# Kernel tuning notes

Hardware: AMD Instinct MI355X
Metric: run time of the kernel (lower is better)

The kernel has to match this reference:

```python
import jax, jax.numpy as jnp
import numpy as np

B, T, H, W = 4, 32, 160, 320
NF, FPF = 8, 8          # num_filters, features_per_filter
SPEED_DIM = 8           # speed_embedding output width
U = 64                  # internal LTC neurons (wiring units)
S = NF * FPF + SPEED_DIM  # 72 sensory inputs
M = 1                   # motor (output) neurons
ODE_UNFOLDS = 6
EPS = 1e-8


def setup_inputs() -> dict:
    key = jax.random.key(0)
    k = jax.random.split(key, 20)
    f32 = jnp.float32
    sp = (H // 8) * (W // 8)  # spatial size per filter after 3 stride-2 convs = 800
    d = {}
    d["input_sequence"] = jax.random.normal(k[0], (B, T, 3, H, W), f32)
    d["speed_sequence"] = jax.random.uniform(k[1], (B, T, 1), f32)
    # conv head params
    d["conv1_w"] = jax.random.normal(k[2], (16, 3, 5, 5), f32) * 0.05
    d["conv1_b"] = jnp.zeros((16,), f32)
    d["conv2_w"] = jax.random.normal(k[3], (32, 16, 5, 5), f32) * 0.05
    d["conv2_b"] = jnp.zeros((32,), f32)
    d["conv3_w"] = jax.random.normal(k[4], (NF, 32, 5, 5), f32) * 0.05
    d["conv3_b"] = jnp.zeros((NF,), f32)
    d["head_w"] = jax.random.normal(k[5], (NF, sp, FPF), f32) * 0.02  # per-filter Linear
    d["head_b"] = jnp.zeros((NF, FPF), f32)
    # speed embedding MLP (Dropout is identity at inference)
    d["se_w1"] = jax.random.normal(k[6], (1, 16), f32) * 0.5
    d["se_b1"] = jnp.zeros((16,), f32)
    d["se_w2"] = jax.random.normal(k[7], (16, SPEED_DIM), f32) * 0.3
    d["se_b2"] = jnp.zeros((SPEED_DIM,), f32)
    # LTC cell params (ncps-style init ranges)
    d["input_w"] = jnp.ones((S,), f32)
    d["input_b"] = jnp.zeros((S,), f32)
    d["gleak"] = jax.random.uniform(k[8], (U,), f32, 0.001, 1.0)
    d["vleak"] = jax.random.uniform(k[9], (U,), f32, -0.2, 0.2)
    d["cm"] = jax.random.uniform(k[10], (U,), f32, 0.4, 0.6)
    d["sigma"] = jax.random.uniform(k[11], (U, U), f32, 3.0, 8.0)
    d["mu"] = jax.random.uniform(k[12], (U, U), f32, 0.3, 0.8)
    d["w_syn"] = jax.random.uniform(k[13], (U, U), f32, 0.001, 1.0)
    d["erev"] = jnp.asarray(jax.random.bernoulli(k[14], 0.5, (U, U)), f32) * 2.0 - 1.0
    d["sensory_sigma"] = jax.random.uniform(k[15], (S, U), f32, 3.0, 8.0)
    d["sensory_mu"] = jax.random.uniform(k[16], (S, U), f32, 0.3, 0.8)
    d["sensory_w"] = jax.random.uniform(k[17], (S, U), f32, 0.001, 1.0)
    d["sensory_erev"] = jnp.asarray(jax.random.bernoulli(k[18], 0.5, (S, U)), f32) * 2.0 - 1.0
    d["output_w"] = jnp.ones((M,), f32)
    d["output_b"] = jnp.zeros((M,), f32)
    return d


def _conv(x, w, b, stride):
    y = jax.lax.conv_general_dilated(
        x, w, (stride, stride), [(2, 2), (2, 2)],
        dimension_numbers=("NCHW", "OIHW", "NCHW"))
    return jax.nn.relu(y + b[None, :, None, None])


def reference(input_sequence, speed_sequence, conv1_w, conv1_b, conv2_w, conv2_b,
              conv3_w, conv3_b, head_w, head_b, se_w1, se_b1, se_w2, se_b2,
              input_w, input_b, gleak, vleak, cm, sigma, mu, w_syn, erev,
              sensory_sigma, sensory_mu, sensory_w, sensory_erev, output_w, output_b):
    Bv, Tv = input_sequence.shape[:2]
    # ---- conv head over all frames at once ----
    x = input_sequence.reshape(Bv * Tv, 3, H, W)
    x = _conv(x, conv1_w, conv1_b, 2)
    x = _conv(x, conv2_w, conv2_b, 2)
    x = _conv(x, conv3_w, conv3_b, 2)          # [N, NF, H/8, W/8]
    x = x.reshape(Bv * Tv, NF, -1)             # [N, NF, 800]
    feats = jnp.einsum("nfp,fpk->nfk", x, head_w) + head_b  # per-filter Linear
    feats = feats.reshape(Bv, Tv, NF * FPF)    # [B, T, 64]
    # global-std normalization (torch .std() uses ddof=1)
    feats = feats / (jnp.std(feats, ddof=1) + 1e-5)
    # ---- speed embedding (vectorized over B,T) ----
    s = speed_sequence[..., :1]                # [B, T, 1]
    emb = jnp.tanh(jax.nn.relu(s @ se_w1 + se_b1) @ se_w2 + se_b2)  # [B, T, 8]
    xs = jnp.concatenate([feats, emb], axis=-1)   # [B, T, S]
    xs = jnp.swapaxes(xs, 0, 1)                   # [T, B, S]
    cm_t = cm * ODE_UNFOLDS  # cm / (elapsed_time / ode_unfolds), elapsed_time = 1.0

    def step(v, x_t):
        inp = x_t * input_w + input_b  # affine input mapping, [B, S]
        s_act = sensory_w * jax.nn.sigmoid((inp[:, :, None] - sensory_mu) * sensory_sigma)  # [B,S,U]
        w_num_s = jnp.sum(s_act * sensory_erev, axis=1)
        w_den_s = jnp.sum(s_act, axis=1)
        for _ in range(ODE_UNFOLDS):  # semi-implicit Euler unfolds
            w_act = w_syn * jax.nn.sigmoid((v[:, :, None] - mu) * sigma)  # [B,U,U]
            w_num = jnp.sum(w_act * erev, axis=1) + w_num_s
            w_den = jnp.sum(w_act, axis=1) + w_den_s
            v = (cm_t * v + gleak * vleak + w_num) / (cm_t + gleak + w_den + EPS)
        out = v[:, :M] * output_w + output_b  # affine output mapping on motor neurons
        return v, (out, v)

    v0 = jnp.zeros((Bv, U), feats.dtype)
    v_last, (outs, hs) = jax.lax.scan(step, v0, xs)
    readout = jnp.swapaxes(outs, 0, 1)  # [B, T, M]
    all_h = jnp.swapaxes(hs, 0, 1)      # [B, T, U]
    return readout, v_last, all_h
```

## Files before the change

### kernel.cpp

```cpp
#include <hip/hip_runtime.h>
#include <math.h>

#define BB 4
#define TT 32
#define NF 8
#define FPF 8
#define SDIM 8
#define UU 64
#define SS 72
#define UNFOLDS 6

typedef short short8 __attribute__((ext_vector_type(8)));
typedef float f32x4 __attribute__((ext_vector_type(4)));
union Frag { uint4 u; short8 s; };

__device__ __forceinline__ float fast_sigmoid(float x) {
    float e = exp2f(-1.44269504f * x);
    return __builtin_amdgcn_rcpf(1.0f + e);
}

__device__ __forceinline__ ushort f2b(float f) {
    union { float f; uint u; } a;
    a.f = f;
    uint u = a.u;
    return (ushort)((u + 0x7FFFu + ((u >> 16) & 1u)) >> 16);
}

__device__ __forceinline__ float bcast_lane(float v, int lane) {
    return __uint_as_float(__builtin_amdgcn_readlane(__float_as_uint(v), lane));
}

__global__ __launch_bounds__(256) void cvt_input(const float* __restrict__ in,
                                                 ushort* __restrict__ outp) {
    int idx = blockIdx.x * 256 + threadIdx.x;
    if (idx >= 128 * 160 * 320) return;
    int x = idx % 320;
    int r = idx / 320;
    int y = r % 160;
    int n = r / 160;
    const float* base = in + ((size_t)n * 3 * 160 + y) * 320 + x;
    float c0 = base[0];
    float c1 = base[160 * 320];
    float c2 = base[2 * 160 * 320];
    uint2 pk;
    pk.x = (uint)f2b(c0) | ((uint)f2b(c1) << 16);
    pk.y = (uint)f2b(c2);
    *(uint2*)(outp + ((size_t)((n * 164 + y + 2) * 328) + (x + 2)) * 4) = pk;
}

template <int HP, int WP, int H, int W, int CH>
__device__ __forceinline__ void halo_body(ushort* __restrict__ buf, int bid) {
    constexpr int TOPBOT = 2 * WP;
    constexpr int SIDE = WP - W;
    constexpr int NH = 2 * TOPBOT + H * SIDE;
    int idx = bid * 256 + threadIdx.x;
    if (idx >= 128 * NH) return;
    int n = idx / NH;
    int h = idx - n * NH;
    int y, x;
    if (h < TOPBOT) {
        y = h / WP;
        x = h % WP;
    } else if (h < 2 * TOPBOT) {
        int hh = h - TOPBOT;
        y = H + 2 + hh / WP;
        x = hh % WP;
    } else {
        int hh = h - 2 * TOPBOT;
        y = 2 + hh / SIDE;
        int xi = hh % SIDE;
        x = (xi < 2) ? xi : (W + xi);
    }
    ushort* p = buf + (((size_t)n * HP + y) * WP + x) * CH;
    if constexpr (CH == 4) {
        *(uint2*)p = make_uint2(0u, 0u);
    } else {
        uint4 z = make_uint4(0u, 0u, 0u, 0u);
#pragma unroll
        for (int i = 0; i < CH / 8; i++) *(uint4*)(p + i * 8) = z;
    }
}
__global__ __launch_bounds__(256) void fill_halo_all(ushort* __restrict__ p1,
                                                     ushort* __restrict__ p2,
                                                     ushort* __restrict__ p3) {
    int bid = blockIdx.x;
    if (bid < 1296)
        halo_body<164, 328, 160, 320, 4>(p1, bid);
    else if (bid < 1296 + 488)
        halo_body<84, 164, 80, 160, 16>(p2, bid - 1296);
    else
        halo_body<44, 84, 40, 80, 32>(p3, bid - 1784);
}

__global__ void wswz1_kernel(const float* __restrict__ w, uint4* __restrict__ o) {
    int i = blockIdx.x * 64 + threadIdx.x;
    if (i >= 5 * 64) return;
    int lane = i & 63, s = i >> 6;
    int oc = lane & 15, q = lane >> 4;
    ushort v[8];
#pragma unroll
    for (int j = 0; j < 8; j++) {
        int k = q * 8 + j;
        int kx = k >> 2, c = k & 3;
        float f = (kx < 5 && c < 3) ? w[((oc * 3 + c) * 5 + s) * 5 + kx] : 0.f;
        v[j] = f2b(f);
    }
    uint4 u;
    u.x = (uint)v[0] | ((uint)v[1] << 16);
    u.y = (uint)v[2] | ((uint)v[3] << 16);
    u.z = (uint)v[4] | ((uint)v[5] << 16);
    u.w = (uint)v[6] | ((uint)v[7] << 16);
    o[i] = u;
}
__global__ void wswz2_kernel(const float* __restrict__ w, uint4* __restrict__ o) {
    int i = blockIdx.x * 64 + threadIdx.x;
    if (i >= 15 * 2 * 64) return;
    int lane = i & 63;
    int ct = (i >> 6) & 1;
    int s = i >> 7;
    int ky = s / 3, kxp = s % 3;
    int oc = ct * 16 + (lane & 15);
    int q = lane >> 4, h = q >> 1;
    int kx = 2 * kxp + h;
    ushort v[8];
#pragma unroll
    for (int j = 0; j < 8; j++) {
        int ch = (q & 1) * 8 + j;
        float f = (kx < 5) ? w[((oc * 16 + ch) * 5 + ky) * 5 + kx] : 0.f;
        v[j] = f2b(f);
    }
    uint4 u;
    u.x = (uint)v[0] | ((uint)v[1] << 16);
    u.y = (uint)v[2] | ((uint)v[3] << 16);
    u.z = (uint)v[4] | ((uint)v[5] << 16);
    u.w = (uint)v[6] | ((uint)v[7] << 16);
    o[i] = u;
}
__global__ void wswz3_kernel(const float* __restrict__ w, uint4* __restrict__ o) {
    int i = blockIdx.x * 64 + threadIdx.x;
    if (i >= 25 * 64) return;
    int lane = i & 63, s = i >> 6;
    int ky = s / 5, kx = s % 5;
    int oc = lane & 15, q = lane >> 4;
    ushort v[8];
#pragma unroll
    for (int j = 0; j < 8; j++) {
        int ch = q * 8 + j;
        float f = (oc < 8) ? w[((oc * 32 + ch) * 5 + ky) * 5 + kx] : 0.f;
        v[j] = f2b(f);
    }
    uint4 u;
    u.x = (uint)v[0] | ((uint)v[1] << 16);
    u.y = (uint)v[2] | ((uint)v[3] << 16);
    u.z = (uint)v[4] | ((uint)v[5] << 16);
    u.w = (uint)v[6] | ((uint)v[7] << 16);
    o[i] = u;
}

__global__ __launch_bounds__(256) void conv1_mfma(const ushort* __restrict__ inp,
                                                  const uint4* __restrict__ wswz,
                                                  const float* __restrict__ bias,
                                                  ushort* __restrict__ outp) {
    const int lane = threadIdx.x & 63;
    const int wid = threadIdx.x >> 6;
    const int col = lane & 15, q = lane >> 4;

    Frag A[5];
#pragma unroll
    for (int s = 0; s < 5; s++) A[s].u = wswz[s * 64 + lane];
    float b0 = bias[q * 4 + 0], b1 = bias[q * 4 + 1], b2 = bias[q * 4 + 2], b3 = bias[q * 4 + 3];

    int gw = blockIdx.x * 4 + wid;
#pragma unroll
    for (int t = 0; t < 4; t++) {
        int p0 = gw * 64 + t * 16;
        int n = p0 / 12800;
        int rem = p0 - n * 12800;
        int oy = rem / 160;
        int ox0 = rem - oy * 160;
        int ox = ox0 + col;
        uint e0 = ((uint)(n * 164 + oy * 2) * 328u + (uint)(ox * 2 + 2 * q)) * 4u;
        f32x4 acc = {0.f, 0.f, 0.f, 0.f};
#pragma unroll
        for (int s = 0; s < 5; s++) {
            Frag B;
            B.u = *(const uint4*)(inp + e0 + (uint)s * (328u * 4u));
            acc = __builtin_amdgcn_mfma_f32_16x16x32_bf16(A[s].s, B.s, acc, 0, 0, 0);
        }
        uint oe = ((uint)(n * 84 + oy + 2) * 164u + (uint)(ox + 2)) * 16u + q * 4u;
        uint2 pk;
        pk.x = (uint)f2b(fmaxf(acc[0] + b0, 0.f)) | ((uint)f2b(fmaxf(acc[1] + b1, 0.f)) << 16);
        pk.y = (uint)f2b(fmaxf(acc[2] + b2, 0.f)) | ((uint)f2b(fmaxf(acc[3] + b3, 0.f)) << 16);
        *(uint2*)(outp + oe) = pk;
    }
}

__global__ __launch_bounds__(256) void conv2_mfma(const ushort* __restrict__ inp,
                                                  const uint4* __restrict__ wswz,
                                                  const float* __restrict__ bias,
                                                  ushort* __restrict__ outp) {
    const int lane = threadIdx.x & 63;
    const int wid = threadIdx.x >> 6;
    const int col = lane & 15, q = lane >> 4;
    const int h = q >> 1, chh = q & 1;

    int gw = blockIdx.x * 4 + wid;
    uint eb[4];
#pragma unroll
    for (int t = 0; t < 4; t++) {
        int p0 = gw * 64 + t * 16;
        int n = p0 / 3200;
        int rem = p0 - n * 3200;
        int oy = rem / 80;
        int ox0 = rem - oy * 80;
        eb[t] = ((uint)(n * 84 + oy * 2) * 164u + (uint)((ox0 + col) * 2 + h)) * 16u + chh * 8u;
    }
    f32x4 acc[4][2];
#pragma unroll
    for (int t = 0; t < 4; t++) {
        acc[t][0] = {0.f, 0.f, 0.f, 0.f};
        acc[t][1] = {0.f, 0.f, 0.f, 0.f};
    }
#pragma unroll
    for (int s = 0; s < 15; s++) {
        const int ky = s / 3, kxp = s % 3;
        Frag A0, A1;
        A0.u = wswz[(s * 2 + 0) * 64 + lane];
        A1.u = wswz[(s * 2 + 1) * 64 + lane];
        const uint d = (uint)ky * (164u * 16u) + (uint)kxp * 32u;
#pragma unroll
        for (int t = 0; t < 4; t++) {
            Frag B;
            B.u = *(const uint4*)(inp + eb[t] + d);
            acc[t][0] = __builtin_amdgcn_mfma_f32_16x16x32_bf16(A0.s, B.s, acc[t][0], 0, 0, 0);
            acc[t][1] = __builtin_amdgcn_mfma_f32_16x16x32_bf16(A1.s, B.s, acc[t][1], 0, 0, 0);
        }
    }
    float ba[2][4];
#pragma unroll
    for (int c = 0; c < 2; c++)
#pragma unroll
        for (int r = 0; r < 4; r++) ba[c][r] = bias[c * 16 + q * 4 + r];
#pragma unroll
    for (int t = 0; t < 4; t++) {
        int p0 = gw * 64 + t * 16;
        int n = p0 / 3200;
        int rem = p0 - n * 3200;
        int oy = rem / 80;
        int ox0 = rem - oy * 80;
        int ox = ox0 + col;
        uint oe = ((uint)(n * 44 + oy + 2) * 84u + (uint)(ox + 2)) * 32u;
#pragma unroll
        for (int c = 0; c < 2; c++) {
            uint2 pk;
            pk.x = (uint)f2b(fmaxf(acc[t][c][0] + ba[c][0], 0.f)) |
                   ((uint)f2b(fmaxf(acc[t][c][1] + ba[c][1], 0.f)) << 16);
            pk.y = (uint)f2b(fmaxf(acc[t][c][2] + ba[c][2], 0.f)) |
                   ((uint)f2b(fmaxf(acc[t][c][3] + ba[c][3], 0.f)) << 16);
            *(uint2*)(outp + oe + (uint)c * 16u + (uint)q * 4u) = pk;
        }
    }
}

__global__ __launch_bounds__(256) void conv3_mfma(const ushort* __restrict__ inp,
                                                  const uint4* __restrict__ wswz,
                                                  const float* __restrict__ bias,
                                                  float* __restrict__ outp) {
    const int lane = threadIdx.x & 63;
    const int wid = threadIdx.x >> 6;
    const int col = lane & 15, q = lane >> 4;

    int gw = blockIdx.x * 4 + wid;
    uint eb[4];
#pragma unroll
    for (int t = 0; t < 4; t++) {
        int p0 = gw * 64 + t * 16;
        int n = p0 / 800;
        int pix = p0 - n * 800 + col;
        int oy = pix / 40;
        int ox = pix - oy * 40;
        eb[t] = ((uint)(n * 44 + oy * 2) * 84u + (uint)(ox * 2)) * 32u + q * 8u;
    }
    f32x4 acc[4];
#pragma unroll
    for (int t = 0; t < 4; t++) acc[t] = {0.f, 0.f, 0.f, 0.f};
#pragma unroll
    for (int s = 0; s < 25; s++) {
        const int ky = s / 5, kx = s % 5;
        Frag A;
        A.u = wswz[s * 64 + lane];
        const uint d = ((uint)ky * 84u + (uint)kx) * 32u;
#pragma unroll
        for (int t = 0; t < 4; t++) {
            Frag B;
            B.u = *(const uint4*)(inp + eb[t] + d);
            acc[t] = __builtin_amdgcn_mfma_f32_16x16x32_bf16(A.s, B.s, acc[t], 0, 0, 0);
        }
    }
    if (q < 2) {
        float b0 = bias[q * 4 + 0], b1 = bias[q * 4 + 1];
        float b2 = bias[q * 4 + 2], b3 = bias[q * 4 + 3];
#pragma unroll
        for (int t = 0; t < 4; t++) {
            int p0 = gw * 64 + t * 16;
            int n = p0 / 800;
            int p = p0 - n * 800 + col;
            float4 v;
            v.x = fmaxf(acc[t][0] + b0, 0.f);
            v.y = fmaxf(acc[t][1] + b1, 0.f);
            v.z = fmaxf(acc[t][2] + b2, 0.f);
            v.w = fmaxf(acc[t][3] + b3, 0.f);
            *(float4*)(outp + ((size_t)n * 800 + p) * 8 + q * 4) = v;
        }
    }
}

__global__ __launch_bounds__(256) void head_kernel(const float* __restrict__ x,
                                                   const float* __restrict__ hw,
                                                   const float* __restrict__ hb,
                                                   float* __restrict__ feats) {
    __shared__ float part[4][64];
    int n = blockIdx.x;
    int tid = threadIdx.x;
    int lane = tid & 63;
    int c = tid >> 6;
    int f = lane >> 3;
    int k = lane & 7;
    const float* xb = x + (size_t)n * 800 * 8 + f;
    const float* wb = hw + ((size_t)f * 800) * FPF + k;
    float acc = 0.0f;
    for (int p = c * 200; p < c * 200 + 200; p++)
        acc = fmaf(xb[(size_t)p * 8], wb[(size_t)p * FPF], acc);
    part[c][lane] = acc;
    __syncthreads();
    if (c == 0)
        feats[n * 64 + lane] = part[0][lane] + part[1][lane] + part[2][lane] + part[3][lane] +
                               hb[lane];
}

__global__ void stats_kernel(const float* __restrict__ feats, float* __restrict__ invstd) {
    __shared__ float s_sum[256], s_sq[256];
    int tid = threadIdx.x;
    float s = 0.0f, q = 0.0f;
    for (int i = tid; i < 8192; i += 256) {
        float x = feats[i];
        s += x;
        q += x * x;
    }
    s_sum[tid] = s;
    s_sq[tid] = q;
    __syncthreads();
    for (int off = 128; off > 0; off >>= 1) {
        if (tid < off) {
            s_sum[tid] += s_sum[tid + off];
            s_sq[tid] += s_sq[tid + off];
        }
        __syncthreads();
    }
    if (tid == 0) {
        float mean = s_sum[0] / 8192.0f;
        float var = (s_sq[0] - 8192.0f * mean * mean) / 8191.0f;
        var = fmaxf(var, 0.0f);
        invstd[0] = 1.0f / (sqrtf(var) + 1e-5f);
    }
}

__global__ void semb_kernel(const float* __restrict__ speed, const float* __restrict__ w1,
                            const float* __restrict__ b1, const float* __restrict__ w2,
                            const float* __restrict__ b2, float* __restrict__ emb) {
    int n = threadIdx.x;
    float s = speed[n];
    float h[16];
#pragma unroll
    for (int j = 0; j < 16; j++) h[j] = fmaxf(fmaf(s, w1[j], b1[j]), 0.0f);
#pragma unroll
    for (int k = 0; k < SDIM; k++) {
        float a = b2[k];
#pragma unroll
        for (int j = 0; j < 16; j++) a = fmaf(h[j], w2[j * SDIM + k], a);
        emb[n * SDIM + k] = tanhf(a);
    }
}

__global__ void sensory_kernel(const float* __restrict__ feats, const float* __restrict__ emb,
                               const float* __restrict__ invstd, const float* __restrict__ inw,
                               const float* __restrict__ inb, const float* __restrict__ ssig,
                               const float* __restrict__ smu, const float* __restrict__ sw,
                               const float* __restrict__ serev, float* __restrict__ wns,
                               float* __restrict__ wds) {
    int bid = blockIdx.x;
    int t = bid >> 2;
    int b = bid & 3;
    int u = threadIdx.x;
    int n = b * TT + t;
    float inv = invstd[0];
    float num = 0.0f, den = 0.0f;
    for (int s = 0; s < SS; s++) {
        float xsv = (s < 64) ? feats[n * 64 + s] * inv : emb[n * SDIM + (s - 64)];
        float inp = fmaf(xsv, inw[s], inb[s]);
        int idx = s * UU + u;
        float x = (inp - smu[idx]) * ssig[idx];
        float act = sw[idx] * fast_sigmoid(x);
        num = fmaf(act, serev[idx], num);
        den += act;
    }
    wns[bid * UU + u] = num;
    wds[bid * UU + u] = den;
}

__global__ __launch_bounds__(512, 1) void scan_kernel(
    const float* __restrict__ wns, const float* __restrict__ wds,
    const float* __restrict__ gleak, const float* __restrict__ vleak,
    const float* __restrict__ cm, const float* __restrict__ sigma,
    const float* __restrict__ mu, const float* __restrict__ wsyn,
    const float* __restrict__ erev, const float* __restrict__ outw,
    const float* __restrict__ outb, float* __restrict__ dout) {
    int b = blockIdx.x;
    int tid = threadIdx.x;
    int u = tid & 63;
    int pc_s = __builtin_amdgcn_readfirstlane(tid >> 6);

    __shared__ float2 pbuf[2][8][64];

    float sA[8], sB[8], wer[8], w_[8];
#pragma unroll
    for (int i = 0; i < 8; i++) {
        int idx = (pc_s * 8 + i) * UU + u;
        float sg = sigma[idx];
        sA[i] = -1.44269504f * sg;
        sB[i] = -sA[i] * mu[idx];
        w_[i] = wsyn[idx];
        wer[i] = w_[i] * erev[idx];
    }
#pragma unroll
    for (int i = 0; i < 8; i++) {
        asm volatile("" : "+v"(sA[i]), "+v"(sB[i]), "+v"(wer[i]), "+v"(w_[i]));
    }
    float cmt = cm[u] * (float)UNFOLDS;
    float gl = gleak[u];
    float glvl = gl * vleak[u];
    float ow = outw[0], ob = outb[0];
    float v = 0.0f;
    int par = 0;

    float num_s = wns[(0 * BB + b) * UU + u];
    float den_s = wds[(0 * BB + b) * UU + u];
    for (int t = 0; t < TT; t++) {
        float nns = 0.f, nds = 0.f;
        if (t + 1 < TT) {
            nns = wns[((t + 1) * BB + b) * UU + u];
            nds = wds[((t + 1) * BB + b) * UU + u];
        }
#pragma unroll
        for (int k = 0; k < UNFOLDS; k++) {
            float num = 0.0f, den = 0.0f;
#pragma unroll
            for (int i = 0; i < 8; i++) {
                float vi = bcast_lane(v, pc_s * 8 + i);
                float e = exp2f(fmaf(vi, sA[i], sB[i]));
                float r = __builtin_amdgcn_rcpf(1.0f + e);
                num = fmaf(wer[i], r, num);
                den = fmaf(w_[i], r, den);
            }
            pbuf[par][pc_s][u] = make_float2(num, den);
            __builtin_amdgcn_sched_barrier(0);
            asm volatile("s_waitcnt lgkmcnt(0)" ::: "memory");
            __builtin_amdgcn_s_barrier();
            asm volatile("" ::: "memory");
            __builtin_amdgcn_sched_barrier(0);
            float nn = num_s, dd = den_s;
#pragma unroll
            for (int j = 0; j < 8; j++) {
                float2 p = pbuf[par][j][u];
                nn += p.x;
                dd += p.y;
            }
            float denom = cmt + gl + dd + 1e-8f;
            v = (fmaf(cmt, v, glvl) + nn) * __builtin_amdgcn_rcpf(denom);
            par ^= 1;
        }
        if (pc_s == 0) {
            dout[384 + (b * TT + t) * UU + u] = v;
            if (u == 0) dout[b * TT + t] = fmaf(v, ow, ob);
            if (t == TT - 1) dout[128 + b * UU + u] = v;
        }
        num_s = nns;
        den_s = nds;
    }
}

extern "C" void kernel_launch(void* const* d_in, const int* in_sizes, int n_in,
                              void* d_out, int out_size, void* d_ws, size_t ws_size,
                              hipStream_t stream) {
    const float* in_seq = (const float*)d_in[0];
    const float* speed = (const float*)d_in[1];
    const float* c1w = (const float*)d_in[2];
    const float* c1b = (const float*)d_in[3];
    const float* c2w = (const float*)d_in[4];
    const float* c2b = (const float*)d_in[5];
    const float* c3w = (const float*)d_in[6];
    const float* c3b = (const float*)d_in[7];
    const float* hw = (const float*)d_in[8];
    const float* hb = (const float*)d_in[9];
    const float* sew1 = (const float*)d_in[10];
    const float* seb1 = (const float*)d_in[11];
    const float* sew2 = (const float*)d_in[12];
    const float* seb2 = (const float*)d_in[13];
    const float* inw = (const float*)d_in[14];
    const float* inb = (const float*)d_in[15];
    const float* gleak = (const float*)d_in[16];
    const float* vleak = (const float*)d_in[17];
    const float* cm = (const float*)d_in[18];
    const float* sigma = (const float*)d_in[19];
    const float* mu = (const float*)d_in[20];
    const float* wsyn = (const float*)d_in[21];
    const float* erev = (const float*)d_in[22];
    const float* ssig = (const float*)d_in[23];
    const float* smu = (const float*)d_in[24];
    const float* sw = (const float*)d_in[25];
    const float* serev = (const float*)d_in[26];
    const float* outw = (const float*)d_in[27];
    const float* outb = (const float*)d_in[28];

    char* ws = (char*)d_ws;
    float* out = (float*)d_out;

    size_t off = 0;
    auto alloc = [&](size_t bytes) {
        size_t o = off;
        off += (bytes + 255) & ~(size_t)255;
        return o;
    };
    ushort* inp1 = (ushort*)(ws + alloc((size_t)128 * 164 * 328 * 4 * 2));
    ushort* c1out = (ushort*)(ws + alloc((size_t)128 * 84 * 164 * 16 * 2));
    ushort* c2out = (ushort*)(ws + alloc((size_t)128 * 44 * 84 * 32 * 2));
    float* c3out = (float*)(ws + alloc((size_t)128 * 800 * 8 * 4));
    float* feats = (float*)(ws + alloc(8192 * 4));
    float* emb = (float*)(ws + alloc(1024 * 4));
    float* invstd = (float*)(ws + alloc(64));
    float* wns = (float*)(ws + alloc(8192 * 4));
    float* wds = (float*)(ws + alloc(8192 * 4));
    uint4* wz1 = (uint4*)(ws + alloc(5 * 64 * 16));
    uint4* wz2 = (uint4*)(ws + alloc(30 * 64 * 16));
    uint4* wz3 = (uint4*)(ws + alloc(25 * 64 * 16));

    wswz1_kernel<<<5, 64, 0, stream>>>(c1w, wz1);
    wswz2_kernel<<<30, 64, 0, stream>>>(c2w, wz2);
    wswz3_kernel<<<25, 64, 0, stream>>>(c3w, wz3);

    fill_halo_all<<<2032, 256, 0, stream>>>(inp1, c1out, c2out);
    cvt_input<<<25600, 256, 0, stream>>>(in_seq, inp1);

    conv1_mfma<<<6400, 256, 0, stream>>>(inp1, wz1, c1b, c1out);
    conv2_mfma<<<1600, 256, 0, stream>>>(c1out, wz2, c2b, c2out);
    conv3_mfma<<<400, 256, 0, stream>>>(c2out, wz3, c3b, c3out);

    head_kernel<<<128, 256, 0, stream>>>(c3out, hw, hb, feats);
    stats_kernel<<<1, 256, 0, stream>>>(feats, invstd);
    semb_kernel<<<1, 128, 0, stream>>>(speed, sew1, seb1, sew2, seb2, emb);

    sensory_kernel<<<TT * BB, 64, 0, stream>>>(feats, emb, invstd, inw, inb, ssig, smu, sw,
                                               serev, wns, wds);

    scan_kernel<<<BB, 512, 0, stream>>>(wns, wds, gleak, vleak, cm, sigma, mu, wsyn, erev,
                                        outw, outb, out);
}
```

Before: 277.2 us.

## Fuse prep kernels into one launch and fold stats/embed/sensory into scan

The weight swizzles, halo fill and input conversion now run as one prep kernel with block-range dispatch. Feature statistics, the speed embedding and the sensory synaptic sums move into the scan kernel, which computes them into shared memory before the recurrence. This cuts eight launches down to two and removes the global round-trips for the intermediate buffers. In exchange, each of the four scan blocks redundantly reduces all of feats and does the sensory work on only four blocks, which may lengthen the serial tail.

```diff
diff --git a/kernel.cpp b/kernel.cpp
--- a/kernel.cpp
+++ b/kernel.cpp
@@ -30,10 +30,8 @@
     return __uint_as_float(__builtin_amdgcn_readlane(__float_as_uint(v), lane));
 }
 
-__global__ __launch_bounds__(256) void cvt_input(const float* __restrict__ in,
-                                                 ushort* __restrict__ outp) {
-    int idx = blockIdx.x * 256 + threadIdx.x;
-    if (idx >= 128 * 160 * 320) return;
+__device__ __forceinline__ void cvt_body(const float* __restrict__ in,
+                                         ushort* __restrict__ outp, int idx) {
     int x = idx % 320;
     int r = idx / 320;
     int y = r % 160;
@@ -80,21 +78,18 @@
         for (int i = 0; i < CH / 8; i++) *(uint4*)(p + i * 8) = z;
     }
 }
-__global__ __launch_bounds__(256) void fill_halo_all(ushort* __restrict__ p1,
-                                                     ushort* __restrict__ p2,
-                                                     ushort* __restrict__ p3) {
-    int bid = blockIdx.x;
-    if (bid < 1296)
-        halo_body<164, 328, 160, 320, 4>(p1, bid);
-    else if (bid < 1296 + 488)
-        halo_body<84, 164, 80, 160, 16>(p2, bid - 1296);
-    else
-        halo_body<44, 84, 40, 80, 32>(p3, bid - 1784);
-}
-
-__global__ void wswz1_kernel(const float* __restrict__ w, uint4* __restrict__ o) {
-    int i = blockIdx.x * 64 + threadIdx.x;
-    if (i >= 5 * 64) return;
+
+__device__ __forceinline__ uint4 pack8(const ushort v[8]) {
+    uint4 u;
+    u.x = (uint)v[0] | ((uint)v[1] << 16);
+    u.y = (uint)v[2] | ((uint)v[3] << 16);
+    u.z = (uint)v[4] | ((uint)v[5] << 16);
+    u.w = (uint)v[6] | ((uint)v[7] << 16);
+    return u;
+}
+
+__device__ __forceinline__ void wswz1_body(const float* __restrict__ w, uint4* __restrict__ o,
+                                           int i) {
     int lane = i & 63, s = i >> 6;
     int oc = lane & 15, q = lane >> 4;
     ushort v[8];
@@ -105,16 +100,10 @@
         float f = (kx < 5 && c < 3) ? w[((oc * 3 + c) * 5 + s) * 5 + kx] : 0.f;
         v[j] = f2b(f);
     }
-    uint4 u;
-    u.x = (uint)v[0] | ((uint)v[1] << 16);
-    u.y = (uint)v[2] | ((uint)v[3] << 16);
-    u.z = (uint)v[4] | ((uint)v[5] << 16);
-    u.w = (uint)v[6] | ((uint)v[7] << 16);
-    o[i] = u;
-}
-__global__ void wswz2_kernel(const float* __restrict__ w, uint4* __restrict__ o) {
-    int i = blockIdx.x * 64 + threadIdx.x;
-    if (i >= 15 * 2 * 64) return;
+    o[i] = pack8(v);
+}
+__device__ __forceinline__ void wswz2_body(const float* __restrict__ w, uint4* __restrict__ o,
+                                           int i) {
     int lane = i & 63;
     int ct = (i >> 6) & 1;
     int s = i >> 7;
@@ -129,16 +118,10 @@
         float f = (kx < 5) ? w[((oc * 16 + ch) * 5 + ky) * 5 + kx] : 0.f;
         v[j] = f2b(f);
     }
-    uint4 u;
-    u.x = (uint)v[0] | ((uint)v[1] << 16);
-    u.y = (uint)v[2] | ((uint)v[3] << 16);
-    u.z = (uint)v[4] | ((uint)v[5] << 16);
-    u.w = (uint)v[6] | ((uint)v[7] << 16);
-    o[i] = u;
-}
-__global__ void wswz3_kernel(const float* __restrict__ w, uint4* __restrict__ o) {
-    int i = blockIdx.x * 64 + threadIdx.x;
-    if (i >= 25 * 64) return;
+    o[i] = pack8(v);
+}
+__device__ __forceinline__ void wswz3_body(const float* __restrict__ w, uint4* __restrict__ o,
+                                           int i) {
     int lane = i & 63, s = i >> 6;
     int ky = s / 5, kx = s % 5;
     int oc = lane & 15, q = lane >> 4;
@@ -149,12 +132,34 @@
         float f = (oc < 8) ? w[((oc * 32 + ch) * 5 + ky) * 5 + kx] : 0.f;
         v[j] = f2b(f);
     }
-    uint4 u;
-    u.x = (uint)v[0] | ((uint)v[1] << 16);
-    u.y = (uint)v[2] | ((uint)v[3] << 16);
-    u.z = (uint)v[4] | ((uint)v[5] << 16);
-    u.w = (uint)v[6] | ((uint)v[7] << 16);
-    o[i] = u;
+    o[i] = pack8(v);
+}
+
+__global__ __launch_bounds__(256) void prep_kernel(
+    const float* __restrict__ in_seq, ushort* __restrict__ inp1, ushort* __restrict__ c1out,
+    ushort* __restrict__ c2out, const float* __restrict__ c1w, const float* __restrict__ c2w,
+    const float* __restrict__ c3w, uint4* __restrict__ wz1, uint4* __restrict__ wz2,
+    uint4* __restrict__ wz3) {
+    int bid = blockIdx.x;
+    if (bid < 25600) {
+        cvt_body(in_seq, inp1, bid * 256 + threadIdx.x);
+    } else if (bid < 25600 + 2032) {
+        int hb = bid - 25600;
+        if (hb < 1296)
+            halo_body<164, 328, 160, 320, 4>(inp1, hb);
+        else if (hb < 1296 + 488)
+            halo_body<84, 164, 80, 160, 16>(c1out, hb - 1296);
+        else
+            halo_body<44, 84, 40, 80, 32>(c2out, hb - 1784);
+    } else {
+        int i = (bid - 27632) * 256 + threadIdx.x;
+        if (i < 320)
+            wswz1_body(c1w, wz1, i);
+        else if (i < 2240)
+            wswz2_body(c2w, wz2, i - 320);
+        else
+            wswz3_body(c3w, wz3, i - 2240);
+    }
 }
 
 __global__ __launch_bounds__(256) void conv1_mfma(const ushort* __restrict__ inp,
@@ -338,78 +343,13 @@
                                hb[lane];
 }
 
-__global__ void stats_kernel(const float* __restrict__ feats, float* __restrict__ invstd) {
-    __shared__ float s_sum[256], s_sq[256];
-    int tid = threadIdx.x;
-    float s = 0.0f, q = 0.0f;
-    for (int i = tid; i < 8192; i += 256) {
-        float x = feats[i];
-        s += x;
-        q += x * x;
-    }
-    s_sum[tid] = s;
-    s_sq[tid] = q;
-    __syncthreads();
-    for (int off = 128; off > 0; off >>= 1) {
-        if (tid < off) {
-            s_sum[tid] += s_sum[tid + off];
-            s_sq[tid] += s_sq[tid + off];
-        }
-        __syncthreads();
-    }
-    if (tid == 0) {
-        float mean = s_sum[0] / 8192.0f;
-        float var = (s_sq[0] - 8192.0f * mean * mean) / 8191.0f;
-        var = fmaxf(var, 0.0f);
-        invstd[0] = 1.0f / (sqrtf(var) + 1e-5f);
-    }
-}
-
-__global__ void semb_kernel(const float* __restrict__ speed, const float* __restrict__ w1,
-                            const float* __restrict__ b1, const float* __restrict__ w2,
-                            const float* __restrict__ b2, float* __restrict__ emb) {
-    int n = threadIdx.x;
-    float s = speed[n];
-    float h[16];
-#pragma unroll
-    for (int j = 0; j < 16; j++) h[j] = fmaxf(fmaf(s, w1[j], b1[j]), 0.0f);
-#pragma unroll
-    for (int k = 0; k < SDIM; k++) {
-        float a = b2[k];
-#pragma unroll
-        for (int j = 0; j < 16; j++) a = fmaf(h[j], w2[j * SDIM + k], a);
-        emb[n * SDIM + k] = tanhf(a);
-    }
-}
-
-__global__ void sensory_kernel(const float* __restrict__ feats, const float* __restrict__ emb,
-                               const float* __restrict__ invstd, const float* __restrict__ inw,
-                               const float* __restrict__ inb, const float* __restrict__ ssig,
-                               const float* __restrict__ smu, const float* __restrict__ sw,
-                               const float* __restrict__ serev, float* __restrict__ wns,
-                               float* __restrict__ wds) {
-    int bid = blockIdx.x;
-    int t = bid >> 2;
-    int b = bid & 3;
-    int u = threadIdx.x;
-    int n = b * TT + t;
-    float inv = invstd[0];
-    float num = 0.0f, den = 0.0f;
-    for (int s = 0; s < SS; s++) {
-        float xsv = (s < 64) ? feats[n * 64 + s] * inv : emb[n * SDIM + (s - 64)];
-        float inp = fmaf(xsv, inw[s], inb[s]);
-        int idx = s * UU + u;
-        float x = (inp - smu[idx]) * ssig[idx];
-        float act = sw[idx] * fast_sigmoid(x);
-        num = fmaf(act, serev[idx], num);
-        den += act;
-    }
-    wns[bid * UU + u] = num;
-    wds[bid * UU + u] = den;
-}
-
-__global__ __launch_bounds__(512, 1) void scan_kernel(
-    const float* __restrict__ wns, const float* __restrict__ wds,
+__global__ __launch_bounds__(512, 1) void scan_fused(
+    const float* __restrict__ feats, const float* __restrict__ speed,
+    const float* __restrict__ sew1, const float* __restrict__ seb1,
+    const float* __restrict__ sew2, const float* __restrict__ seb2,
+    const float* __restrict__ inw, const float* __restrict__ inb,
+    const float* __restrict__ ssig, const float* __restrict__ smu,
+    const float* __restrict__ sw, const float* __restrict__ serev,
     const float* __restrict__ gleak, const float* __restrict__ vleak,
     const float* __restrict__ cm, const float* __restrict__ sigma,
     const float* __restrict__ mu, const float* __restrict__ wsyn,
@@ -420,6 +360,9 @@
     int u = tid & 63;
     int pc_s = __builtin_amdgcn_readfirstlane(tid >> 6);
 
+    __shared__ float2 red[512];
+    __shared__ float2 sens[TT][UU];
+    __shared__ float embsh[TT][SDIM];
     __shared__ float2 pbuf[2][8][64];
 
     float sA[8], sB[8], wer[8], w_[8];
@@ -436,6 +379,61 @@
     for (int i = 0; i < 8; i++) {
         asm volatile("" : "+v"(sA[i]), "+v"(sB[i]), "+v"(wer[i]), "+v"(w_[i]));
     }
+
+    float s = 0.0f, q = 0.0f;
+    for (int i = tid; i < 8192; i += 512) {
+        float x = feats[i];
+        s += x;
+        q += x * x;
+    }
+    red[tid] = make_float2(s, q);
+    __syncthreads();
+    for (int off = 256; off > 0; off >>= 1) {
+        if (tid < off) {
+            float2 o = red[tid + off];
+            float2 m = red[tid];
+            red[tid] = make_float2(m.x + o.x, m.y + o.y);
+        }
+        __syncthreads();
+    }
+    float2 SQ = red[0];
+    float mean = SQ.x / 8192.0f;
+    float var = fmaxf((SQ.y - 8192.0f * mean * mean) / 8191.0f, 0.0f);
+    float inv = 1.0f / (sqrtf(var) + 1e-5f);
+
+    if (tid < 256) {
+        int t = tid >> 3, k = tid & 7;
+        float sp = speed[b * TT + t];
+        float a = seb2[k];
+#pragma unroll
+        for (int j = 0; j < 16; j++) {
+            float h = fmaxf(fmaf(sp, sew1[j], seb1[j]), 0.0f);
+            a = fmaf(h, sew2[j * SDIM + k], a);
+        }
+        embsh[t][k] = tanhf(a);
+    }
+    __syncthreads();
+
+#pragma unroll
+    for (int p = 0; p < 4; p++) {
+        int pair = p * 512 + tid;
+        int t = pair >> 6;
+        int uu = pair & 63;
+        int n = b * TT + t;
+        float num = 0.0f, den = 0.0f;
+        for (int ss = 0; ss < SS; ss++) {
+            float xsv = (ss < 64) ? feats[n * 64 + ss] * inv : embsh[t][ss - 64];
+            float inp = fmaf(xsv, inw[ss], inb[ss]);
+            int idx = ss * UU + uu;
+            float x = (inp - smu[idx]) * ssig[idx];
+            float act = sw[idx] * fast_sigmoid(x);
+            num = fmaf(act, serev[idx], num);
+            den += act;
+        }
+        sens[t][uu] = make_float2(num, den);
+    }
+    __syncthreads();
+
     float cmt = cm[u] * (float)UNFOLDS;
     float gl = gleak[u];
     float glvl = gl * vleak[u];
@@ -443,14 +441,9 @@
     float v = 0.0f;
     int par = 0;
 
-    float num_s = wns[(0 * BB + b) * UU + u];
-    float den_s = wds[(0 * BB + b) * UU + u];
     for (int t = 0; t < TT; t++) {
-        float nns = 0.f, nds = 0.f;
-        if (t + 1 < TT) {
-            nns = wns[((t + 1) * BB + b) * UU + u];
-            nds = wds[((t + 1) * BB + b) * UU + u];
-        }
+        float2 nsd = sens[t][u];
+        float num_s = nsd.x, den_s = nsd.y;
 #pragma unroll
         for (int k = 0; k < UNFOLDS; k++) {
             float num = 0.0f, den = 0.0f;
@@ -484,8 +477,6 @@
             if (u == 0) dout[b * TT + t] = fmaf(v, ow, ob);
             if (t == TT - 1) dout[128 + b * UU + u] = v;
         }
-        num_s = nns;
-        den_s = nds;
     }
 }
 
@@ -536,32 +527,20 @@
     ushort* c2out = (ushort*)(ws + alloc((size_t)128 * 44 * 84 * 32 * 2));
     float* c3out = (float*)(ws + alloc((size_t)128 * 800 * 8 * 4));
     float* feats = (float*)(ws + alloc(8192 * 4));
-    float* emb = (float*)(ws + alloc(1024 * 4));
-    float* invstd = (float*)(ws + alloc(64));
-    float* wns = (float*)(ws + alloc(8192 * 4));
-    float* wds = (float*)(ws + alloc(8192 * 4));
     uint4* wz1 = (uint4*)(ws + alloc(5 * 64 * 16));
     uint4* wz2 = (uint4*)(ws + alloc(30 * 64 * 16));
     uint4* wz3 = (uint4*)(ws + alloc(25 * 64 * 16));
 
-    wswz1_kernel<<<5, 64, 0, stream>>>(c1w, wz1);
-    wswz2_kernel<<<30, 64, 0, stream>>>(c2w, wz2);
-    wswz3_kernel<<<25, 64, 0, stream>>>(c3w, wz3);
-
-    fill_halo_all<<<2032, 256, 0, stream>>>(inp1, c1out, c2out);
-    cvt_input<<<25600, 256, 0, stream>>>(in_seq, inp1);
+    prep_kernel<<<27647, 256, 0, stream>>>(in_seq, inp1, c1out, c2out, c1w, c2w, c3w, wz1,
+                                           wz2, wz3);
 
     conv1_mfma<<<6400, 256, 0, stream>>>(inp1, wz1, c1b, c1out);
     conv2_mfma<<<1600, 256, 0, stream>>>(c1out, wz2, c2b, c2out);
     conv3_mfma<<<400, 256, 0, stream>>>(c2out, wz3, c3b, c3out);
 
     head_kernel<<<128, 256, 0, stream>>>(c3out, hw, hb, feats);
-    stats_kernel<<<1, 256, 0, stream>>>(feats, invstd);
-    semb_kernel<<<1, 128, 0, stream>>>(speed, sew1, seb1, sew2, seb2, emb);
-
-    sensory_kernel<<<TT * BB, 64, 0, stream>>>(feats, emb, invstd, inw, inb, ssig, smu, sw,
-                                               serev, wns, wds);
-
-    scan_kernel<<<BB, 512, 0, stream>>>(wns, wds, gleak, vleak, cm, sigma, mu, wsyn, erev,
-                                        outw, outb, out);
-}
+
+    scan_fused<<<BB, 512, 0, stream>>>(feats, speed, sew1, seb1, sew2, seb2, inw, inb, ssig,
+                                       smu, sw, serev, gleak, vleak, cm, sigma, mu, wsyn,
+                                       erev, outw, outb, out);
+}
```

Result: slower. 301.0 us (+8.6%).
